# Kernel tuning notes

Measured on AMD Instinct MI355X. Metric: run time of the kernel, lower is better.

## Reference

```python
import jax, jax.numpy as jnp
import numpy as np

B, N, F_IN, F_OUT = 8, 2048, 64, 64
ALPHA = 0.2
NEG = -9e15


def setup_inputs() -> dict:
    key = jax.random.key(0)
    k1, k2, k3, k4 = jax.random.split(key, 4)
    h = jax.random.normal(k1, (B, N, F_IN), dtype=jnp.float32)
    adj = jax.random.randint(k2, (N, N), 0, 2).astype(jnp.float32)
    W = jax.random.normal(k3, (F_OUT, F_IN), dtype=jnp.float32) * 0.05
    a = jax.random.normal(k4, (2 * F_OUT,), dtype=jnp.float32) * 0.05
    return {"h": h, "adj": adj, "W": W, "a": a}


def reference(h, adj, W, a):
    # Wh = h @ W^T  : [B, N, F_OUT]
    Wh = jnp.einsum("bnf,of->bno", h, W)
    # a([Wh_i, Wh_j]) decomposes exactly into a1.Wh_i + a2.Wh_j
    e1 = Wh @ a[:F_OUT]          # [B, N] contribution of source node i
    e2 = Wh @ a[F_OUT:]          # [B, N] contribution of target node j
    e = jax.nn.leaky_relu(e1[:, :, None] + e2[:, None, :], negative_slope=ALPHA)
    att = jnp.where(adj[None, :, :] > 0, e, NEG)
    att = jax.nn.softmax(att, axis=-1)   # [B, N, N]
    h_prime = jnp.einsum("bij,bjo->bio", att, Wh)
    return jax.nn.elu(h_prime)
```

## Files before the change

### kernel.cpp

```cpp
#include <hip/hip_runtime.h>
#include <hip/hip_bf16.h>
#include <math.h>


#define NN 2048
#define BB 8

typedef __attribute__((ext_vector_type(8))) short s8v;
typedef __attribute__((ext_vector_type(4))) float f4v;

static __device__ __forceinline__ unsigned pk_bf16(float lo, float hi) {
  __hip_bfloat162 t = __float22bfloat162_rn(float2{lo, hi});
  return *(unsigned*)&t;
}

__global__ __launch_bounds__(256, 2) void k_pre(
    const float* __restrict__ adj, const float* __restrict__ h,
    const float* __restrict__ W, const float* __restrict__ a,
    unsigned long long* __restrict__ adjq, unsigned short* __restrict__ whswz,
    float2* __restrict__ e1pn, float2* __restrict__ e2pn) {
  const int t = threadIdx.x, lane = t & 63, w = t >> 6;

  if (blockIdx.x >= 512) {
    const int bid = blockIdx.x - 512;
    const int row = bid * 2 + (w >> 1);
    const int half = w & 1;
    const float* ar = adj + (size_t)row * NN + half * 1024;
    unsigned long long* aq = adjq + row * 32 + half * 16;
    #pragma unroll
    for (int it = 0; it < 16; ++it) {
      unsigned long long m = __ballot(ar[it * 64 + lane] > 0.f);
      if (lane == 0) aq[it] = m;
    }
    return;
  }

  __shared__ __align__(16) float hs[32][68];
  const int rowBase = blockIdx.x * 32;
  const int b = rowBase >> 11, n0 = rowBase & (NN - 1);
  const int jt = n0 >> 6, ks = (n0 >> 5) & 1;

  float wr[64];
  #pragma unroll
  for (int k = 0; k < 16; ++k)
    *(f4v*)&wr[k * 4] = *(const f4v*)&W[lane * 64 + k * 4];

  #pragma unroll
  for (int qq = 0; qq < 2; ++qq) {
    const int idx = t + 256 * qq;
    const int r = idx >> 4, c = (idx & 15) * 4;
    *(f4v*)&hs[r][c] = *(const f4v*)&h[(size_t)(rowBase + r) * 64 + c];
  }
  const float a1v = a[lane], a2v = a[64 + lane];
  __syncthreads();

  const int r0 = w * 8;
  float acc[8];
  #pragma unroll
  for (int rr = 0; rr < 8; ++rr) acc[rr] = 0.f;
  #pragma unroll
  for (int f4i = 0; f4i < 16; ++f4i) {
    f4v hv[8];
    #pragma unroll
    for (int rr = 0; rr < 8; ++rr)
      hv[rr] = *(const f4v*)&hs[r0 + rr][f4i * 4];
    #pragma unroll
    for (int x = 0; x < 4; ++x) {
      const float wv = wr[f4i * 4 + x];
      #pragma unroll
      for (int rr = 0; rr < 8; ++rr) acc[rr] = fmaf(hv[rr][x], wv, acc[rr]);
    }
  }

  {
    union { s8v v; unsigned u[4]; } cv;
    cv.u[0] = pk_bf16(acc[0], acc[1]);
    cv.u[1] = pk_bf16(acc[2], acc[3]);
    cv.u[2] = pk_bf16(acc[4], acc[5]);
    cv.u[3] = pk_bf16(acc[6], acc[7]);
    unsigned short* dst = whswz + ((size_t)b << 17) + (jt << 12) +
                          ((((lane >> 4) << 1) + ks) << 9) +
                          ((w * 16 + (lane & 15)) << 3);
    *(s8v*)dst = cv.v;
  }

  float s1[8], s2[8];
  #pragma unroll
  for (int rr = 0; rr < 8; ++rr) { s1[rr] = acc[rr] * a1v; s2[rr] = acc[rr] * a2v; }
  #pragma unroll
  for (int m = 1; m < 64; m <<= 1)
    #pragma unroll
    for (int rr = 0; rr < 8; ++rr) {
      s1[rr] += __shfl_xor(s1[rr], m);
      s2[rr] += __shfl_xor(s2[rr], m);
    }
  #pragma unroll
  for (int rr = 0; rr < 8; ++rr) {
    const float2 f1 = {__expf(s1[rr]), __expf(0.2f * s1[rr])};
    const float2 f2 = {__expf(s2[rr]), __expf(0.2f * s2[rr])};
    if (lane == 0) {
      e1pn[rowBase + r0 + rr] = f1;
      e2pn[rowBase + r0 + rr] = f2;
    }
  }
}

__global__ __launch_bounds__(256, 4) void k_attn(
    const unsigned long long* __restrict__ adjq,
    const unsigned short* __restrict__ whswz,
    const float2* __restrict__ e1png, const float2* __restrict__ e2png,
    float* __restrict__ out) {
  __shared__ __align__(16) float2 e2s[NN];
  __shared__ __align__(16) float pc[4][16][68];
  __shared__ float ls[4][16];

  const int t = threadIdx.x, lane = t & 63, w = t >> 6;
  const int q = lane >> 4, l15 = lane & 15;
  const int b = blockIdx.y;
  const int i0 = blockIdx.x * 16;
  const size_t bN = (size_t)b * NN;

  #pragma unroll
  for (int kk = 0; kk < 4; ++kk) {
    const int idx4 = t + 256 * kk;
    ((f4v*)e2s)[idx4] = ((const f4v*)(e2png + bN))[idx4];
  }

  const float2 e1f = e1png[bN + i0 + l15];
  const float E1p = e1f.x, E1n = e1f.y;
  const unsigned long long* arow = adjq + (size_t)(i0 + l15) * 32 + w * 8;
  const unsigned short* tb = whswz + ((size_t)b << 17) + ((size_t)(w * 8) << 12);

  f4v accA[4], accB[4];
  #pragma unroll
  for (int s = 0; s < 4; ++s) {
    accA[s] = f4v{0.f, 0.f, 0.f, 0.f};
    accB[s] = f4v{0.f, 0.f, 0.f, 0.f};
  }
  float psum = 0.f;

  __syncthreads();

  #pragma unroll
  for (int k = 0; k < 4; ++k) {
    s8v bfA[8], bfB[8];
    const unsigned short* gA = tb + (k << 12) + (lane << 3);
    const unsigned short* gB = gA + (4 << 12);
    #pragma unroll
    for (int f = 0; f < 8; ++f) {
      bfA[f] = *(const s8v*)(gA + (f << 9));
      bfB[f] = *(const s8v*)(gB + (f << 9));
    }
    const unsigned long long amA = arow[k], amB = arow[k + 4];

    s8v afA[2], afB[2];
    #pragma unroll
    for (int ch = 0; ch < 2; ++ch) {
      const unsigned long long am = ch ? amB : amA;
      const int j0 = (w * 8 + k + (ch ? 4 : 0)) << 6;
      #pragma unroll
      for (int ks = 0; ks < 2; ++ks) {
        const unsigned bits = (unsigned)(am >> (ks * 32 + q * 8)) & 0xffu;
        const int jb = j0 + ks * 32 + q * 8;
        float p[8];
        #pragma unroll
        for (int jj = 0; jj < 8; ++jj) {
          const float2 e2f = e2s[jb + jj];
          const float mp = E1p * e2f.x;
          const float mn = E1n * e2f.y;
          float pv = mp > 1.f ? mp : mn;
          pv = ((bits >> jj) & 1u) ? pv : 0.f;
          p[jj] = pv;
          psum += pv;
        }
        union { s8v v; unsigned u[4]; } cv;
        cv.u[0] = pk_bf16(p[0], p[1]);
        cv.u[1] = pk_bf16(p[2], p[3]);
        cv.u[2] = pk_bf16(p[4], p[5]);
        cv.u[3] = pk_bf16(p[6], p[7]);
        if (ch) afB[ks] = cv.v; else afA[ks] = cv.v;
      }
    }

    #pragma unroll
    for (int s = 0; s < 4; ++s) {
      accA[s] = __builtin_amdgcn_mfma_f32_16x16x32_bf16(afA[0], bfA[s * 2 + 0], accA[s], 0, 0, 0);
      accA[s] = __builtin_amdgcn_mfma_f32_16x16x32_bf16(afA[1], bfA[s * 2 + 1], accA[s], 0, 0, 0);
      accB[s] = __builtin_amdgcn_mfma_f32_16x16x32_bf16(afB[0], bfB[s * 2 + 0], accB[s], 0, 0, 0);
      accB[s] = __builtin_amdgcn_mfma_f32_16x16x32_bf16(afB[1], bfB[s * 2 + 1], accB[s], 0, 0, 0);
    }
  }

  f4v acc[4];
  #pragma unroll
  for (int s = 0; s < 4; ++s) acc[s] = accA[s] + accB[s];
  psum += __shfl_xor(psum, 16);
  psum += __shfl_xor(psum, 32);
  if (lane < 16) ls[w][lane] = psum;
  #pragma unroll
  for (int s = 0; s < 4; ++s)
    #pragma unroll
    for (int r = 0; r < 4; ++r)
      pc[w][q * 4 + r][s * 16 + l15] = acc[s][r];
  __syncthreads();

  const int row = t >> 4, c0 = (t & 15) * 4;
  f4v sum = *(const f4v*)&pc[0][row][c0];
  #pragma unroll
  for (int j = 1; j < 4; ++j) sum += *(const f4v*)&pc[j][row][c0];
  const float rsum = ls[0][row] + ls[1][row] + ls[2][row] + ls[3][row];
  f4v o;
  #pragma unroll
  for (int x = 0; x < 4; ++x) {
    float v = sum[x] / rsum;
    o[x] = v > 0.f ? v : expm1f(v);
  }
  *(f4v*)&out[(bN + i0 + row) * 64 + c0] = o;
}

extern "C" void kernel_launch(void* const* d_in, const int* in_sizes, int n_in,
                              void* d_out, int out_size, void* d_ws, size_t ws_size,
                              hipStream_t stream) {
  (void)in_sizes; (void)n_in; (void)out_size; (void)ws_size;
  const float* h   = (const float*)d_in[0];
  const float* adj = (const float*)d_in[1];
  const float* W   = (const float*)d_in[2];
  const float* a   = (const float*)d_in[3];
  float* outp = (float*)d_out;

  unsigned short* whswz = (unsigned short*)d_ws;
  float2* e1pn = (float2*)((char*)d_ws + (size_t)BB * 64 * NN * 2);
  float2* e2pn = e1pn + (size_t)BB * NN;
  unsigned long long* adjq = (unsigned long long*)(e2pn + (size_t)BB * NN);

  k_pre<<<1536, 256, 0, stream>>>(adj, h, W, a, adjq, whswz, e1pn, e2pn);
  k_attn<<<dim3(NN / 16, BB), 256, 0, stream>>>(adjq, whswz, e1pn, e2pn, outp);
}
```

Baseline: 99.61 us.

## Switch attention kernel to 32x32 MFMA tiles with packed bf16 e2 factors

Reworks the attention kernel so each block handles 32 query rows with 8 waves using 32x32x16 bf16 MFMA, instead of 16 rows with 4 waves using 16x16x32. The Wh layout written by the preprocessing kernel is re-swizzled to match the new B-operand fragment layout. The e2 exponentials are packed as two bf16 values in one dword, which halves the shared-memory staging and LDS reads, and the e2 buffer shares an LDS union with the reduction buffer. The grid is flattened with batch in the low bits. This trades some precision in e2 and a larger block for fewer, larger MFMA ops and better reuse of the Wh operand loads.

New measurement: 97.88 us. No clear change (-1.7%).

```diff
diff --git a/kernel.cpp b/kernel.cpp
--- a/kernel.cpp
+++ b/kernel.cpp
@@ -8,17 +8,24 @@
 
 typedef __attribute__((ext_vector_type(8))) short s8v;
 typedef __attribute__((ext_vector_type(4))) float f4v;
+typedef __attribute__((ext_vector_type(16))) float f16v;
+typedef __attribute__((ext_vector_type(4))) unsigned u4v;
 
 static __device__ __forceinline__ unsigned pk_bf16(float lo, float hi) {
   __hip_bfloat162 t = __float22bfloat162_rn(float2{lo, hi});
   return *(unsigned*)&t;
+}
+static __device__ __forceinline__ unsigned short bf16rne(float x) {
+  union { float f; unsigned u; } c; c.f = x;
+  unsigned r = c.u + 0x7FFFu + ((c.u >> 16) & 1u);
+  return (unsigned short)(r >> 16);
 }
 
 __global__ __launch_bounds__(256, 2) void k_pre(
     const float* __restrict__ adj, const float* __restrict__ h,
     const float* __restrict__ W, const float* __restrict__ a,
     unsigned long long* __restrict__ adjq, unsigned short* __restrict__ whswz,
-    float2* __restrict__ e1pn, float2* __restrict__ e2pn) {
+    float2* __restrict__ e1pn, unsigned* __restrict__ e2pk) {
   const int t = threadIdx.x, lane = t & 63, w = t >> 6;
 
   if (blockIdx.x >= 512) {
@@ -38,7 +45,6 @@
   __shared__ __align__(16) float hs[32][68];
   const int rowBase = blockIdx.x * 32;
   const int b = rowBase >> 11, n0 = rowBase & (NN - 1);
-  const int jt = n0 >> 6, ks = (n0 >> 5) & 1;
 
   float wr[64];
   #pragma unroll
@@ -78,9 +84,10 @@
     cv.u[1] = pk_bf16(acc[2], acc[3]);
     cv.u[2] = pk_bf16(acc[4], acc[5]);
     cv.u[3] = pk_bf16(acc[6], acc[7]);
-    unsigned short* dst = whswz + ((size_t)b << 17) + (jt << 12) +
-                          ((((lane >> 4) << 1) + ks) << 9) +
-                          ((w * 16 + (lane & 15)) << 3);
+    const int jc = (n0 + w * 8) >> 4;
+    const int oh = lane >> 5;
+    const int lp = ((w & 1) << 5) + (lane & 31);
+    unsigned short* dst = whswz + ((size_t)b << 17) + (jc << 10) + (oh << 9) + (lp << 3);
     *(s8v*)dst = cv.v;
   }
 
@@ -96,119 +103,114 @@
     }
   #pragma unroll
   for (int rr = 0; rr < 8; ++rr) {
-    const float2 f1 = {__expf(s1[rr]), __expf(0.2f * s1[rr])};
-    const float2 f2 = {__expf(s2[rr]), __expf(0.2f * s2[rr])};
     if (lane == 0) {
-      e1pn[rowBase + r0 + rr] = f1;
-      e2pn[rowBase + r0 + rr] = f2;
-    }
-  }
-}
-
-__global__ __launch_bounds__(256, 4) void k_attn(
+      e1pn[rowBase + rr + r0] = float2{__expf(s1[rr]), __expf(0.2f * s1[rr])};
+      e2pk[rowBase + rr + r0] =
+          (unsigned)bf16rne(__expf(s2[rr])) |
+          ((unsigned)bf16rne(__expf(0.2f * s2[rr])) << 16);
+    }
+  }
+}
+
+__global__ __launch_bounds__(512, 4) void k_attn(
     const unsigned long long* __restrict__ adjq,
     const unsigned short* __restrict__ whswz,
-    const float2* __restrict__ e1png, const float2* __restrict__ e2png,
+    const float2* __restrict__ e1png, const unsigned* __restrict__ e2pkg,
     float* __restrict__ out) {
-  __shared__ __align__(16) float2 e2s[NN];
-  __shared__ __align__(16) float pc[4][16][68];
-  __shared__ float ls[4][16];
+  union SM {
+    unsigned e2bf[NN];
+    float pc[8][32][68];
+  };
+  __shared__ __align__(16) SM sm;
+  __shared__ float ls[8][32];
 
   const int t = threadIdx.x, lane = t & 63, w = t >> 6;
-  const int q = lane >> 4, l15 = lane & 15;
-  const int b = blockIdx.y;
-  const int i0 = blockIdx.x * 16;
+  const int m32 = lane & 31, kh = lane >> 5;
+  const int g = blockIdx.x;
+  const int b = g & 7;
+  const int i0 = (g >> 3) << 5;
   const size_t bN = (size_t)b * NN;
 
-  #pragma unroll
-  for (int kk = 0; kk < 4; ++kk) {
-    const int idx4 = t + 256 * kk;
-    ((f4v*)e2s)[idx4] = ((const f4v*)(e2png + bN))[idx4];
-  }
-
-  const float2 e1f = e1png[bN + i0 + l15];
+  ((u4v*)sm.e2bf)[t] = ((const u4v*)(e2pkg + bN))[t];
+
+  const float2 e1f = e1png[bN + i0 + m32];
   const float E1p = e1f.x, E1n = e1f.y;
-  const unsigned long long* arow = adjq + (size_t)(i0 + l15) * 32 + w * 8;
-  const unsigned short* tb = whswz + ((size_t)b << 17) + ((size_t)(w * 8) << 12);
-
-  f4v accA[4], accB[4];
-  #pragma unroll
-  for (int s = 0; s < 4; ++s) {
-    accA[s] = f4v{0.f, 0.f, 0.f, 0.f};
-    accB[s] = f4v{0.f, 0.f, 0.f, 0.f};
-  }
+  const unsigned long long* arow = adjq + (size_t)(i0 + m32) * 32 + w * 4;
+  const unsigned short* wb = whswz + ((size_t)b << 17);
+
+  f16v acc0, acc1;
+  #pragma unroll
+  for (int r = 0; r < 16; ++r) { acc0[r] = 0.f; acc1[r] = 0.f; }
   float psum = 0.f;
 
-  __syncthreads();
-
-  #pragma unroll
-  for (int k = 0; k < 4; ++k) {
-    s8v bfA[8], bfB[8];
-    const unsigned short* gA = tb + (k << 12) + (lane << 3);
-    const unsigned short* gB = gA + (4 << 12);
-    #pragma unroll
-    for (int f = 0; f < 8; ++f) {
-      bfA[f] = *(const s8v*)(gA + (f << 9));
-      bfB[f] = *(const s8v*)(gB + (f << 9));
-    }
-    const unsigned long long amA = arow[k], amB = arow[k + 4];
-
-    s8v afA[2], afB[2];
-    #pragma unroll
-    for (int ch = 0; ch < 2; ++ch) {
-      const unsigned long long am = ch ? amB : amA;
-      const int j0 = (w * 8 + k + (ch ? 4 : 0)) << 6;
-      #pragma unroll
-      for (int ks = 0; ks < 2; ++ks) {
-        const unsigned bits = (unsigned)(am >> (ks * 32 + q * 8)) & 0xffu;
-        const int jb = j0 + ks * 32 + q * 8;
-        float p[8];
-        #pragma unroll
-        for (int jj = 0; jj < 8; ++jj) {
-          const float2 e2f = e2s[jb + jj];
-          const float mp = E1p * e2f.x;
-          const float mn = E1n * e2f.y;
-          float pv = mp > 1.f ? mp : mn;
-          pv = ((bits >> jj) & 1u) ? pv : 0.f;
-          p[jj] = pv;
-          psum += pv;
-        }
-        union { s8v v; unsigned u[4]; } cv;
-        cv.u[0] = pk_bf16(p[0], p[1]);
-        cv.u[1] = pk_bf16(p[2], p[3]);
-        cv.u[2] = pk_bf16(p[4], p[5]);
-        cv.u[3] = pk_bf16(p[6], p[7]);
-        if (ch) afB[ks] = cv.v; else afA[ks] = cv.v;
-      }
-    }
-
-    #pragma unroll
-    for (int s = 0; s < 4; ++s) {
-      accA[s] = __builtin_amdgcn_mfma_f32_16x16x32_bf16(afA[0], bfA[s * 2 + 0], accA[s], 0, 0, 0);
-      accA[s] = __builtin_amdgcn_mfma_f32_16x16x32_bf16(afA[1], bfA[s * 2 + 1], accA[s], 0, 0, 0);
-      accB[s] = __builtin_amdgcn_mfma_f32_16x16x32_bf16(afB[0], bfB[s * 2 + 0], accB[s], 0, 0, 0);
-      accB[s] = __builtin_amdgcn_mfma_f32_16x16x32_bf16(afB[1], bfB[s * 2 + 1], accB[s], 0, 0, 0);
-    }
-  }
-
-  f4v acc[4];
-  #pragma unroll
-  for (int s = 0; s < 4; ++s) acc[s] = accA[s] + accB[s];
-  psum += __shfl_xor(psum, 16);
+  auto pgen = [&](u4v e0, u4v e1, unsigned bits) -> s8v {
+    float p[8];
+    #pragma unroll
+    for (int e = 0; e < 8; ++e) {
+      const unsigned dw = e < 4 ? e0[e] : e1[e - 4];
+      const float E2p = __uint_as_float(dw << 16);
+      const float E2n = __uint_as_float(dw & 0xffff0000u);
+      const float mp = E1p * E2p;
+      const float mn = E1n * E2n;
+      float pv = mp > 1.f ? mp : mn;
+      pv = ((bits >> e) & 1u) ? pv : 0.f;
+      psum += pv;
+      p[e] = pv;
+    }
+    union { s8v v; unsigned u[4]; } cv;
+    cv.u[0] = pk_bf16(p[0], p[1]);
+    cv.u[1] = pk_bf16(p[2], p[3]);
+    cv.u[2] = pk_bf16(p[4], p[5]);
+    cv.u[3] = pk_bf16(p[6], p[7]);
+    return cv.v;
+  };
+
+  __syncthreads();
+
+  unsigned long long am = 0;
+  #pragma unroll
+  for (int it = 0; it < 8; ++it) {
+    const int jcl = it * 2;
+    const int jcA = w * 16 + jcl, jcB = jcA + 1;
+    const s8v bA0 = *(const s8v*)(wb + (jcA << 10) + (lane << 3));
+    const s8v bA1 = *(const s8v*)(wb + (jcA << 10) + 512 + (lane << 3));
+    const s8v bB0 = *(const s8v*)(wb + (jcB << 10) + (lane << 3));
+    const s8v bB1 = *(const s8v*)(wb + (jcB << 10) + 512 + (lane << 3));
+    if ((it & 1) == 0) am = arow[it >> 1];
+    const u4v eA0 = *(const u4v*)&sm.e2bf[(jcA << 4) + (kh << 3)];
+    const u4v eA1 = *(const u4v*)&sm.e2bf[(jcA << 4) + (kh << 3) + 4];
+    const u4v eB0 = *(const u4v*)&sm.e2bf[(jcB << 4) + (kh << 3)];
+    const u4v eB1 = *(const u4v*)&sm.e2bf[(jcB << 4) + (kh << 3) + 4];
+
+    const unsigned bitsA = (unsigned)(am >> (((jcl)&3) * 16 + kh * 8)) & 0xffu;
+    const unsigned bitsB = (unsigned)(am >> (((jcl + 1) & 3) * 16 + kh * 8)) & 0xffu;
+    const s8v afA = pgen(eA0, eA1, bitsA);
+    const s8v afB = pgen(eB0, eB1, bitsB);
+
+    acc0 = __builtin_amdgcn_mfma_f32_32x32x16_bf16(afA, bA0, acc0, 0, 0, 0);
+    acc1 = __builtin_amdgcn_mfma_f32_32x32x16_bf16(afA, bA1, acc1, 0, 0, 0);
+    acc0 = __builtin_amdgcn_mfma_f32_32x32x16_bf16(afB, bB0, acc0, 0, 0, 0);
+    acc1 = __builtin_amdgcn_mfma_f32_32x32x16_bf16(afB, bB1, acc1, 0, 0, 0);
+  }
+
   psum += __shfl_xor(psum, 32);
-  if (lane < 16) ls[w][lane] = psum;
-  #pragma unroll
-  for (int s = 0; s < 4; ++s)
-    #pragma unroll
-    for (int r = 0; r < 4; ++r)
-      pc[w][q * 4 + r][s * 16 + l15] = acc[s][r];
+  __syncthreads();
+  if (lane < 32) ls[w][lane] = psum;
+  #pragma unroll
+  for (int r = 0; r < 16; ++r) {
+    const int row = (r & 3) + 8 * (r >> 2) + 4 * kh;
+    sm.pc[w][row][m32] = acc0[r];
+    sm.pc[w][row][32 + m32] = acc1[r];
+  }
   __syncthreads();
 
   const int row = t >> 4, c0 = (t & 15) * 4;
-  f4v sum = *(const f4v*)&pc[0][row][c0];
-  #pragma unroll
-  for (int j = 1; j < 4; ++j) sum += *(const f4v*)&pc[j][row][c0];
-  const float rsum = ls[0][row] + ls[1][row] + ls[2][row] + ls[3][row];
+  f4v sum = *(const f4v*)&sm.pc[0][row][c0];
+  #pragma unroll
+  for (int j = 1; j < 8; ++j) sum += *(const f4v*)&sm.pc[j][row][c0];
+  float rsum = ls[0][row];
+  #pragma unroll
+  for (int j = 1; j < 8; ++j) rsum += ls[j][row];
   f4v o;
   #pragma unroll
   for (int x = 0; x < 4; ++x) {
@@ -230,9 +232,9 @@
 
   unsigned short* whswz = (unsigned short*)d_ws;
   float2* e1pn = (float2*)((char*)d_ws + (size_t)BB * 64 * NN * 2);
-  float2* e2pn = e1pn + (size_t)BB * NN;
-  unsigned long long* adjq = (unsigned long long*)(e2pn + (size_t)BB * NN);
-
-  k_pre<<<1536, 256, 0, stream>>>(adj, h, W, a, adjq, whswz, e1pn, e2pn);
-  k_attn<<<dim3(NN / 16, BB), 256, 0, stream>>>(adjq, whswz, e1pn, e2pn, outp);
-}
+  unsigned* e2pk = (unsigned*)(e1pn + (size_t)BB * NN);
+  unsigned long long* adjq = (unsigned long long*)(e2pk + (size_t)BB * NN);
+
+  k_pre<<<1536, 256, 0, stream>>>(adj, h, W, a, adjq, whswz, e1pn, e2pk);
+  k_attn<<<512, 512, 0, stream>>>(adjq, whswz, e1pn, e2pk, outp);
+}
```
